# Optimization experiments

Hardware: AMD Instinct MI355X
Metric: run time of the kernel (lower is better)

The kernel has to match this reference:

```python
import math
import jax, jax.numpy as jnp
import numpy as np

IMG_SIZE = 2048
STRIDE = 8
NUM_CLASSES = 80
TOPK = 1000
CONF_THRESH = 0.05
NMS_THRESH = 0.6
CTR_CLAMP = 32.0
SCALE_CLAMP = math.log(1000.0 / 16)
ANCHOR_SIZES = np.array([[32,32],[64,32],[32,64],[64,64],[128,64],[64,128],[128,128],[256,128],[128,256]], dtype=np.float32)


def make_anchors():
    fmp = IMG_SIZE // STRIDE  # 256
    yy, xx = np.meshgrid(np.arange(fmp), np.arange(fmp), indexing='ij')
    xy = (np.stack([xx, yy], axis=-1).reshape(-1, 2).astype(np.float32) + 0.5) * STRIDE  # [fmp*fmp, 2]
    na = ANCHOR_SIZES.shape[0]
    xy = np.repeat(xy[:, None, :], na, axis=1)           # [fmp*fmp, na, 2]
    wh = np.tile(ANCHOR_SIZES[None, :, :], (fmp * fmp, 1, 1))  # [fmp*fmp, na, 2]
    return jnp.asarray(np.concatenate([xy, wh], axis=-1).reshape(-1, 4))  # [M, 4]


def setup_inputs() -> dict:
    key = jax.random.key(0)
    k1, k2 = jax.random.split(key)
    M = (IMG_SIZE // STRIDE) ** 2 * ANCHOR_SIZES.shape[0]
    cls_pred = jax.random.normal(k1, (M, NUM_CLASSES), dtype=jnp.float32) * 2.0 - 2.0
    reg_pred = jax.random.normal(k2, (M, 4), dtype=jnp.float32) * 0.5
    anchor_boxes = make_anchors()
    return {"cls_pred": cls_pred, "reg_pred": reg_pred, "anchor_boxes": anchor_boxes}


def decode_boxes(anchors, reg):
    # anchors, reg: [N, 4] (cx, cy, w, h) / (dx, dy, dw, dh)
    ctr_off = jnp.clip(reg[..., :2] * anchors[..., 2:], -CTR_CLAMP, CTR_CLAMP)
    ctr = anchors[..., :2] + ctr_off
    wh = anchors[..., 2:] * jnp.exp(jnp.minimum(reg[..., 2:], SCALE_CLAMP))
    return jnp.concatenate([ctr - 0.5 * wh, ctr + 0.5 * wh], axis=-1)


def iou_matrix(boxes):
    # boxes: [N, 4] x1y1x2y2 -> [N, N] IoU, matching the numpy NMS math
    x1, y1, x2, y2 = boxes[:, 0], boxes[:, 1], boxes[:, 2], boxes[:, 3]
    areas = (x2 - x1) * (y2 - y1)
    xx1 = jnp.maximum(x1[:, None], x1[None, :])
    yy1 = jnp.maximum(y1[:, None], y1[None, :])
    xx2 = jnp.minimum(x2[:, None], x2[None, :])
    yy2 = jnp.minimum(y2[:, None], y2[None, :])
    w = jnp.maximum(1e-10, xx2 - xx1)
    h = jnp.maximum(1e-10, yy2 - yy1)
    inter = w * h
    return inter / (areas[:, None] + areas[None, :] - inter + 1e-10)


def reference(cls_pred, reg_pred, anchor_boxes):
    # per-anchor best class score/label
    probs = jax.nn.sigmoid(cls_pred)                 # [M, C]
    scores_all = jnp.max(probs, axis=-1)             # [M]
    labels_all = jnp.argmax(probs, axis=-1)          # [M]
    # top-k filtering (scores sorted descending)
    scores, idx = jax.lax.top_k(scores_all, TOPK)    # [K]
    labels = labels_all[idx]
    reg = reg_pred[idx]
    anch = anchor_boxes[idx]
    # decode + normalize
    bboxes = jnp.clip(decode_boxes(anch, reg) / IMG_SIZE, 0.0, 1.0)  # [K, 4]
    valid = scores >= CONF_THRESH                    # conf filter as mask (fixed shape)
    # per-class greedy NMS: candidates are score-sorted, so greedy order = index order
    iou = iou_matrix(bboxes)                         # [K, K]
    same_cls = labels[:, None] == labels[None, :]    # [K, K]
    suppress_mat = (iou > NMS_THRESH) & same_cls     # j suppresses i if kept, same class, earlier
    idx_range = jnp.arange(TOPK)

    def body(i, keep):
        earlier_kept_overlap = jnp.any(keep & suppress_mat[:, i] & (idx_range < i))
        return keep.at[i].set(valid[i] & ~earlier_kept_overlap)

    keep = jax.lax.fori_loop(0, TOPK, body, jnp.zeros(TOPK, dtype=bool))
    return bboxes, scores, labels, keep
```

## Files before the change

kernel.cpp:

```cpp
#include <hip/hip_runtime.h>
#include <math.h>

#define M_ANCH   589824
#define NCLS     80
#define TOPK_N   1000
#define CAND_CAP 4096
#define NREP     16
#define NBIN     8192
#define KSHIFT   19

#define SCALE_CLAMP_F 4.135166556742356f
#define INV_IMG       (1.0f/2048.0f)

#define WS_H1R     0
#define WS_CNT     524288
#define WS_GBIN    524292
#define WS_MEMSET  524296
#define WS_CAND    524544
#define WS_BOXES   557312
#define WS_LABELS  573312
#define WS_VALID   577312
#define WS_SUP     581376
#define WS_MKEYS   712704

__device__ __forceinline__ unsigned fmap(unsigned b) {
    return (b & 0x80000000u) ? ~b : (b | 0x80000000u);
}
__device__ __forceinline__ unsigned funmap(unsigned k) {
    return (k & 0x80000000u) ? (k ^ 0x80000000u) : ~k;
}

__global__ __launch_bounds__(256) void k_rowmax(const float* __restrict__ cls,
                                                unsigned* __restrict__ mkeys,
                                                unsigned* __restrict__ h1r) {
    __shared__ float    cmax[256 * 21];
    __shared__ unsigned lh[NBIN / 2];
    int t = threadIdx.x;
    for (int b = t; b < NBIN / 2; b += 256) lh[b] = 0;

    const float4* p = (const float4*)cls + (size_t)blockIdx.x * (256 * 20);
#pragma unroll
    for (int i = 0; i < 20; ++i) {
        float4 v = p[i * 256 + t];
        float c = fmaxf(fmaxf(v.x, v.y), fmaxf(v.z, v.w));
        int cid = i * 256 + t;
        int row = cid / 20;
        int j   = cid - row * 20;
        cmax[row * 21 + j] = c;
    }
    __syncthreads();

    const float* rp = &cmax[t * 21];
    float m = -INFINITY;
#pragma unroll
    for (int j = 0; j < 20; ++j) m = fmaxf(m, rp[j]);
    unsigned key = fmap(__float_as_uint(m));
    mkeys[blockIdx.x * 256 + t] = key;
    unsigned bin = key >> KSHIFT;
    atomicAdd(&lh[bin >> 1], 1u << ((bin & 1) << 4));
    __syncthreads();

    unsigned rep = (blockIdx.x & (NREP - 1)) * NBIN;
    for (int b2 = t; b2 < NBIN / 2; b2 += 256) {
        unsigned c = lh[b2];
        unsigned c0 = c & 0xFFFFu, c1 = c >> 16;
        if (c0) atomicAdd(&h1r[rep + 2 * b2], c0);
        if (c1) atomicAdd(&h1r[rep + 2 * b2 + 1], c1);
    }
}

__global__ __launch_bounds__(1024) void k_find(const unsigned* __restrict__ h1r,
                                               unsigned* __restrict__ gbin) {
    __shared__ unsigned hist[NBIN];
    __shared__ unsigned csum[256];
    int t = threadIdx.x;
    for (int b = t; b < NBIN; b += 1024) {
        unsigned s = 0;
#pragma unroll
        for (int r = 0; r < NREP; ++r) s += h1r[r * NBIN + b];
        hist[b] = s;
    }
    __syncthreads();
    if (t < 256) {
        unsigned cs = 0;
        for (int k = 0; k < 32; ++k) cs += hist[t * 32 + k];
        csum[t] = cs;
    }
    __syncthreads();
    if (t == 0) {
        unsigned cum = 0, above = 0;
        int C = 0;
        for (int c = 255; c >= 0; --c) {
            if (cum + csum[c] >= TOPK_N || c == 0) { C = c; above = cum; break; }
            cum += csum[c];
        }
        int B = C * 32;
        unsigned cum2 = above;
        for (int b = C * 32 + 31; b >= C * 32; --b) {
            cum2 += hist[b];
            if (cum2 >= TOPK_N) { B = b; break; }
            if (b == C * 32) B = b;
        }
        *gbin = (B >= 1) ? (unsigned)(B - 1) : 0u;
    }
}

__global__ __launch_bounds__(256) void k_gather(const uint4* __restrict__ mk4,
                                                const unsigned* __restrict__ gbin,
                                                unsigned* __restrict__ cnt,
                                                unsigned long long* __restrict__ cand) {
    int tid = blockIdx.x * 256 + threadIdx.x;
    unsigned gb = *gbin;
    uint4 a = mk4[tid * 2];
    uint4 b4 = mk4[tid * 2 + 1];
    unsigned keys[8] = {a.x, a.y, a.z, a.w, b4.x, b4.y, b4.z, b4.w};
    int lc = 0;
    unsigned sel[8];
#pragma unroll
    for (int q = 0; q < 8; ++q)
        if ((keys[q] >> KSHIFT) >= gb) sel[lc++] = (unsigned)q;
    if (lc) {
        unsigned base = atomicAdd(cnt, (unsigned)lc);
        for (int q = 0; q < lc; ++q) {
            unsigned pos = base + (unsigned)q;
            if (pos < CAND_CAP) {
                unsigned i = (unsigned)tid * 8u + sel[q];
                float m = __uint_as_float(funmap(keys[sel[q]]));
                float e = (float)exp(-(double)m);
                float sc = 1.0f / (1.0f + e);
                cand[pos] = ((unsigned long long)__float_as_uint(sc) << 32)
                            | (unsigned)(~i);
            }
        }
    }
}

__global__ __launch_bounds__(256) void k_rank_decode(const unsigned* __restrict__ cnt,
                                                     const unsigned long long* __restrict__ cand,
                                                     const float* __restrict__ cls,
                                                     const float* __restrict__ reg,
                                                     const float* __restrict__ anch,
                                                     float* __restrict__ out,
                                                     float4* __restrict__ boxes_ws,
                                                     int* __restrict__ lab_ws,
                                                     int* __restrict__ val_ws) {
    __shared__ unsigned long long sh[CAND_CAP];
    int t = threadIdx.x;
    unsigned n = *cnt;
    if (n > CAND_CAP) n = CAND_CAP;
    for (int k = t; k < (int)n; k += 256) sh[k] = cand[k];
    __syncthreads();
    int k = blockIdx.x * 256 + t;
    if (k >= (int)n) return;
    unsigned long long key = sh[k];
    int rank = 0;
    for (int j = 0; j < (int)n; ++j) rank += (sh[j] > key) ? 1 : 0;
    if (rank >= TOPK_N) return;
    int r = rank;
    unsigned idx = ~(unsigned)(key & 0xFFFFFFFFull);
    float sc = __uint_as_float((unsigned)(key >> 32));
    const float4* rowp = (const float4*)(cls + (size_t)idx * NCLS);
    float best = -INFINITY;
    int lbl = 0;
#pragma unroll
    for (int c4 = 0; c4 < 20; ++c4) {
        float4 v = rowp[c4];
        if (v.x > best) { best = v.x; lbl = c4 * 4; }
        if (v.y > best) { best = v.y; lbl = c4 * 4 + 1; }
        if (v.z > best) { best = v.z; lbl = c4 * 4 + 2; }
        if (v.w > best) { best = v.w; lbl = c4 * 4 + 3; }
    }
    float4 rg = ((const float4*)reg)[idx];
    float4 an = ((const float4*)anch)[idx];
    float ox = fminf(fmaxf(rg.x * an.z, -32.0f), 32.0f);
    float oy = fminf(fmaxf(rg.y * an.w, -32.0f), 32.0f);
    float cx = an.x + ox, cy = an.y + oy;
    float w = an.z * expf(fminf(rg.z, SCALE_CLAMP_F));
    float h = an.w * expf(fminf(rg.w, SCALE_CLAMP_F));
    float x1 = fminf(fmaxf((cx - 0.5f * w) * INV_IMG, 0.0f), 1.0f);
    float y1 = fminf(fmaxf((cy - 0.5f * h) * INV_IMG, 0.0f), 1.0f);
    float x2 = fminf(fmaxf((cx + 0.5f * w) * INV_IMG, 0.0f), 1.0f);
    float y2 = fminf(fmaxf((cy + 0.5f * h) * INV_IMG, 0.0f), 1.0f);
    out[r * 4 + 0] = x1;
    out[r * 4 + 1] = y1;
    out[r * 4 + 2] = x2;
    out[r * 4 + 3] = y2;
    out[4 * TOPK_N + r] = sc;
    out[5 * TOPK_N + r] = (float)lbl;
    boxes_ws[r] = make_float4(x1, y1, x2, y2);
    lab_ws[r] = lbl;
    val_ws[r] = (sc >= 0.05f) ? 1 : 0;
}

__global__ __launch_bounds__(64) void k_sup(const float4* __restrict__ boxes,
                                            const int* __restrict__ labs,
                                            unsigned long long* __restrict__ supT) {
    int i = blockIdx.x;
    int lane = threadIdx.x;
    int cmax = i >> 6;
    float4 bi = boxes[i];
    float ai = (bi.z - bi.x) * (bi.w - bi.y);
    int li = labs[i];
    for (int c = 0; c <= cmax; ++c) {
        int j = c * 64 + lane;
        bool bit = false;
        if (j < TOPK_N) {
            float4 bj = boxes[j];
            float aj = (bj.z - bj.x) * (bj.w - bj.y);
            float xx1 = fmaxf(bi.x, bj.x), yy1 = fmaxf(bi.y, bj.y);
            float xx2 = fminf(bi.z, bj.z), yy2 = fminf(bi.w, bj.w);
            float w = fmaxf(1e-10f, xx2 - xx1);
            float h = fmaxf(1e-10f, yy2 - yy1);
            float inter = w * h;
            float iou = inter / (ai + aj - inter + 1e-10f);
            bit = (iou > 0.6f) && (labs[j] == li);
        }
        unsigned long long ball = __ballot(bit);
        if (lane == 0) supT[(size_t)c * 1024 + i] = ball;
    }
}

__global__ __launch_bounds__(64) void k_nms(const unsigned long long* __restrict__ supT,
                                            const int* __restrict__ val,
                                            float* __restrict__ out_keep) {
    int lane = threadIdx.x;
    unsigned long long kw[16];
    unsigned long long lowmask = (lane == 0) ? 0ull : (~0ull >> (64 - lane));
#pragma unroll
    for (int c = 0; c < 16; ++c) {
        int b = c * 64 + lane;
        bool inb = (b < TOPK_N);
        unsigned long long tmp[16];
#pragma unroll
        for (int w = 0; w <= c; ++w)
            tmp[w] = inb ? supT[(size_t)w * 1024 + b] : 0ull;
        bool v = inb && (val[b] != 0);
        bool ext = false;
#pragma unroll
        for (int w = 0; w < c; ++w) ext = ext || ((tmp[w] & kw[w]) != 0ull);
        unsigned long long m = tmp[c];
        unsigned long long inchunk = m & lowmask;
        bool mykeep;
        if (__ballot(inchunk != 0ull) == 0ull) {
            mykeep = v && !ext;
        } else {
            mykeep = false;
            for (int i = 0; i < 64; ++i) {
                unsigned long long ball = __ballot(mykeep);
                if (lane == i) mykeep = v && !ext && ((ball & inchunk) == 0ull);
            }
        }
        unsigned long long ball2 = __ballot(mykeep);
        kw[c] = ball2;
        if (inb) out_keep[b] = ((ball2 >> lane) & 1ull) ? 1.0f : 0.0f;
    }
}

extern "C" void kernel_launch(void* const* d_in, const int* in_sizes, int n_in,
                              void* d_out, int out_size, void* d_ws, size_t ws_size,
                              hipStream_t stream) {
    const float* cls  = (const float*)d_in[0];
    const float* reg  = (const float*)d_in[1];
    const float* anch = (const float*)d_in[2];
    float* out = (float*)d_out;
    char* ws = (char*)d_ws;

    unsigned* h1r  = (unsigned*)(ws + WS_H1R);
    unsigned* cnt  = (unsigned*)(ws + WS_CNT);
    unsigned* gbin = (unsigned*)(ws + WS_GBIN);
    unsigned long long* cand = (unsigned long long*)(ws + WS_CAND);
    float4* boxes = (float4*)(ws + WS_BOXES);
    int* labs     = (int*)(ws + WS_LABELS);
    int* valid    = (int*)(ws + WS_VALID);
    unsigned long long* supT = (unsigned long long*)(ws + WS_SUP);
    unsigned* mkeys = (unsigned*)(ws + WS_MKEYS);

    hipMemsetAsync(ws, 0, WS_MEMSET, stream);

    k_rowmax<<<M_ANCH / 256, 256, 0, stream>>>(cls, mkeys, h1r);
    k_find  <<<1, 1024, 0, stream>>>(h1r, gbin);
    k_gather<<<M_ANCH / (256 * 8), 256, 0, stream>>>((const uint4*)mkeys, gbin, cnt, cand);
    k_rank_decode<<<CAND_CAP / 256, 256, 0, stream>>>(cnt, cand, cls, reg, anch,
                                                      out, boxes, labs, valid);
    k_sup   <<<TOPK_N, 64, 0, stream>>>(boxes, labs, supT);
    k_nms   <<<1, 64, 0, stream>>>(supT, valid, out + 6 * TOPK_N);
}
```

Before: 368.6 us.

## Fuse histogram reduce/find and suppress/NMS via last-block ticket pattern

The single-block histogram reduction becomes a 32-block parallel reduction, and the last block to finish (picked with an atomic ticket) runs the threshold search. The suppression-matrix and greedy NMS kernels are merged the same way, with four rows per 256-thread block and the last block doing the NMS. This removes a kernel launch boundary in each pair and spreads the histogram reduction across many CUs. The cost is extra thread fences, an atomic counter that must be zeroed each call, and a serial tail run by whichever block finishes last.

```diff
diff --git a/kernel.cpp b/kernel.cpp
--- a/kernel.cpp
+++ b/kernel.cpp
@@ -15,13 +15,16 @@
 #define WS_H1R     0
 #define WS_CNT     524288
 #define WS_GBIN    524292
-#define WS_MEMSET  524296
+#define WS_TICK1   524296
+#define WS_TICK2   524300
+#define WS_MEMSET  524304
 #define WS_CAND    524544
 #define WS_BOXES   557312
 #define WS_LABELS  573312
 #define WS_VALID   577312
 #define WS_SUP     581376
 #define WS_MKEYS   712704
+#define WS_HRED    3072000
 
 __device__ __forceinline__ unsigned fmap(unsigned b) {
     return (b & 0x80000000u) ? ~b : (b | 0x80000000u);
@@ -69,19 +72,29 @@
     }
 }
 
-__global__ __launch_bounds__(1024) void k_find(const unsigned* __restrict__ h1r,
-                                               unsigned* __restrict__ gbin) {
+__global__ __launch_bounds__(256) void k_red_find(const unsigned* __restrict__ h1r,
+                                                  unsigned* __restrict__ hred,
+                                                  unsigned* __restrict__ ticket,
+                                                  unsigned* __restrict__ gbin) {
     __shared__ unsigned hist[NBIN];
     __shared__ unsigned csum[256];
+    __shared__ unsigned amLast;
     int t = threadIdx.x;
-    for (int b = t; b < NBIN; b += 1024) {
-        unsigned s = 0;
-#pragma unroll
-        for (int r = 0; r < NREP; ++r) s += h1r[r * NBIN + b];
-        hist[b] = s;
-    }
-    __syncthreads();
-    if (t < 256) {
+    int b = blockIdx.x * 256 + t;
+    unsigned s = 0;
+#pragma unroll
+    for (int r = 0; r < NREP; ++r) s += h1r[r * NBIN + b];
+    hred[b] = s;
+    __threadfence();
+    __syncthreads();
+    if (t == 0) amLast = (atomicAdd(ticket, 1u) == (NBIN / 256 - 1)) ? 1u : 0u;
+    __syncthreads();
+    if (!amLast) return;
+    __threadfence();
+
+    for (int i = t; i < NBIN; i += 256) hist[i] = hred[i];
+    __syncthreads();
+    {
         unsigned cs = 0;
         for (int k = 0; k < 32; ++k) cs += hist[t * 32 + k];
         csum[t] = cs;
@@ -96,10 +109,10 @@
         }
         int B = C * 32;
         unsigned cum2 = above;
-        for (int b = C * 32 + 31; b >= C * 32; --b) {
-            cum2 += hist[b];
-            if (cum2 >= TOPK_N) { B = b; break; }
-            if (b == C * 32) B = b;
+        for (int b2 = C * 32 + 31; b2 >= C * 32; --b2) {
+            cum2 += hist[b2];
+            if (cum2 >= TOPK_N) { B = b2; break; }
+            if (b2 == C * 32) B = b2;
         }
         *gbin = (B >= 1) ? (unsigned)(B - 1) : 0u;
     }
@@ -192,67 +205,77 @@
     val_ws[r] = (sc >= 0.05f) ? 1 : 0;
 }
 
-__global__ __launch_bounds__(64) void k_sup(const float4* __restrict__ boxes,
-                                            const int* __restrict__ labs,
-                                            unsigned long long* __restrict__ supT) {
-    int i = blockIdx.x;
-    int lane = threadIdx.x;
-    int cmax = i >> 6;
-    float4 bi = boxes[i];
-    float ai = (bi.z - bi.x) * (bi.w - bi.y);
-    int li = labs[i];
-    for (int c = 0; c <= cmax; ++c) {
-        int j = c * 64 + lane;
-        bool bit = false;
-        if (j < TOPK_N) {
-            float4 bj = boxes[j];
-            float aj = (bj.z - bj.x) * (bj.w - bj.y);
-            float xx1 = fmaxf(bi.x, bj.x), yy1 = fmaxf(bi.y, bj.y);
-            float xx2 = fminf(bi.z, bj.z), yy2 = fminf(bi.w, bj.w);
-            float w = fmaxf(1e-10f, xx2 - xx1);
-            float h = fmaxf(1e-10f, yy2 - yy1);
-            float inter = w * h;
-            float iou = inter / (ai + aj - inter + 1e-10f);
-            bit = (iou > 0.6f) && (labs[j] == li);
-        }
-        unsigned long long ball = __ballot(bit);
-        if (lane == 0) supT[(size_t)c * 1024 + i] = ball;
-    }
-}
-
-__global__ __launch_bounds__(64) void k_nms(const unsigned long long* __restrict__ supT,
-                                            const int* __restrict__ val,
-                                            float* __restrict__ out_keep) {
-    int lane = threadIdx.x;
-    unsigned long long kw[16];
-    unsigned long long lowmask = (lane == 0) ? 0ull : (~0ull >> (64 - lane));
-#pragma unroll
-    for (int c = 0; c < 16; ++c) {
-        int b = c * 64 + lane;
-        bool inb = (b < TOPK_N);
-        unsigned long long tmp[16];
-#pragma unroll
-        for (int w = 0; w <= c; ++w)
-            tmp[w] = inb ? supT[(size_t)w * 1024 + b] : 0ull;
-        bool v = inb && (val[b] != 0);
-        bool ext = false;
-#pragma unroll
-        for (int w = 0; w < c; ++w) ext = ext || ((tmp[w] & kw[w]) != 0ull);
-        unsigned long long m = tmp[c];
-        unsigned long long inchunk = m & lowmask;
-        bool mykeep;
-        if (__ballot(inchunk != 0ull) == 0ull) {
-            mykeep = v && !ext;
-        } else {
-            mykeep = false;
-            for (int i = 0; i < 64; ++i) {
-                unsigned long long ball = __ballot(mykeep);
-                if (lane == i) mykeep = v && !ext && ((ball & inchunk) == 0ull);
+__global__ __launch_bounds__(256) void k_sup_nms(const float4* __restrict__ boxes,
+                                                 const int* __restrict__ labs,
+                                                 unsigned long long* __restrict__ supT,
+                                                 unsigned* __restrict__ ticket,
+                                                 const int* __restrict__ val,
+                                                 float* __restrict__ out_keep) {
+    __shared__ unsigned amLast;
+    int t = threadIdx.x;
+    int i = blockIdx.x * 4 + (t >> 6);
+    int lane = t & 63;
+    if (i < TOPK_N) {
+        int cmax = i >> 6;
+        float4 bi = boxes[i];
+        float ai = (bi.z - bi.x) * (bi.w - bi.y);
+        int li = labs[i];
+        for (int c = 0; c <= cmax; ++c) {
+            int j = c * 64 + lane;
+            bool bit = false;
+            if (j < TOPK_N) {
+                float4 bj = boxes[j];
+                float aj = (bj.z - bj.x) * (bj.w - bj.y);
+                float xx1 = fmaxf(bi.x, bj.x), yy1 = fmaxf(bi.y, bj.y);
+                float xx2 = fminf(bi.z, bj.z), yy2 = fminf(bi.w, bj.w);
+                float w = fmaxf(1e-10f, xx2 - xx1);
+                float h = fmaxf(1e-10f, yy2 - yy1);
+                float inter = w * h;
+                float iou = inter / (ai + aj - inter + 1e-10f);
+                bit = (iou > 0.6f) && (labs[j] == li);
             }
-        }
-        unsigned long long ball2 = __ballot(mykeep);
-        kw[c] = ball2;
-        if (inb) out_keep[b] = ((ball2 >> lane) & 1ull) ? 1.0f : 0.0f;
+            unsigned long long ball = __ballot(bit);
+            if (lane == 0) supT[(size_t)c * 1024 + i] = ball;
+        }
+    }
+    __threadfence();
+    __syncthreads();
+    if (t == 0) amLast = (atomicAdd(ticket, 1u) == (TOPK_N / 4 - 1)) ? 1u : 0u;
+    __syncthreads();
+    if (!amLast) return;
+    __threadfence();
+
+    if (t < 64) {
+        unsigned long long kw[16];
+        unsigned long long lowmask = (lane == 0) ? 0ull : (~0ull >> (64 - lane));
+#pragma unroll
+        for (int c = 0; c < 16; ++c) {
+            int b = c * 64 + lane;
+            bool inb = (b < TOPK_N);
+            unsigned long long tmp[16];
+#pragma unroll
+            for (int w = 0; w <= c; ++w)
+                tmp[w] = inb ? supT[(size_t)w * 1024 + b] : 0ull;
+            bool v = inb && (val[b] != 0);
+            bool ext = false;
+#pragma unroll
+            for (int w = 0; w < c; ++w) ext = ext || ((tmp[w] & kw[w]) != 0ull);
+            unsigned long long m = tmp[c];
+            unsigned long long inchunk = m & lowmask;
+            bool mykeep;
+            if (__ballot(inchunk != 0ull) == 0ull) {
+                mykeep = v && !ext;
+            } else {
+                mykeep = false;
+                for (int ii = 0; ii < 64; ++ii) {
+                    unsigned long long ball = __ballot(mykeep);
+                    if (lane == ii) mykeep = v && !ext && ((ball & inchunk) == 0ull);
+                }
+            }
+            unsigned long long ball2 = __ballot(mykeep);
+            kw[c] = ball2;
+            if (inb) out_keep[b] = ((ball2 >> lane) & 1ull) ? 1.0f : 0.0f;
+        }
     }
 }
 
@@ -265,23 +288,26 @@
     float* out = (float*)d_out;
     char* ws = (char*)d_ws;
 
-    unsigned* h1r  = (unsigned*)(ws + WS_H1R);
-    unsigned* cnt  = (unsigned*)(ws + WS_CNT);
-    unsigned* gbin = (unsigned*)(ws + WS_GBIN);
+    unsigned* h1r   = (unsigned*)(ws + WS_H1R);
+    unsigned* cnt   = (unsigned*)(ws + WS_CNT);
+    unsigned* gbin  = (unsigned*)(ws + WS_GBIN);
+    unsigned* tick1 = (unsigned*)(ws + WS_TICK1);
+    unsigned* tick2 = (unsigned*)(ws + WS_TICK2);
     unsigned long long* cand = (unsigned long long*)(ws + WS_CAND);
     float4* boxes = (float4*)(ws + WS_BOXES);
     int* labs     = (int*)(ws + WS_LABELS);
     int* valid    = (int*)(ws + WS_VALID);
     unsigned long long* supT = (unsigned long long*)(ws + WS_SUP);
     unsigned* mkeys = (unsigned*)(ws + WS_MKEYS);
+    unsigned* hred  = (unsigned*)(ws + WS_HRED);
 
     hipMemsetAsync(ws, 0, WS_MEMSET, stream);
 
-    k_rowmax<<<M_ANCH / 256, 256, 0, stream>>>(cls, mkeys, h1r);
-    k_find  <<<1, 1024, 0, stream>>>(h1r, gbin);
-    k_gather<<<M_ANCH / (256 * 8), 256, 0, stream>>>((const uint4*)mkeys, gbin, cnt, cand);
+    k_rowmax  <<<M_ANCH / 256, 256, 0, stream>>>(cls, mkeys, h1r);
+    k_red_find<<<NBIN / 256, 256, 0, stream>>>(h1r, hred, tick1, gbin);
+    k_gather  <<<M_ANCH / (256 * 8), 256, 0, stream>>>((const uint4*)mkeys, gbin, cnt, cand);
     k_rank_decode<<<CAND_CAP / 256, 256, 0, stream>>>(cnt, cand, cls, reg, anch,
                                                       out, boxes, labs, valid);
-    k_sup   <<<TOPK_N, 64, 0, stream>>>(boxes, labs, supT);
-    k_nms   <<<1, 64, 0, stream>>>(supT, valid, out + 6 * TOPK_N);
-}
+    k_sup_nms <<<TOPK_N / 4, 256, 0, stream>>>(boxes, labs, supT, tick2,
+                                               valid, out + 6 * TOPK_N);
+}
```

New measurement: 368.8 us. About the same (+0.1%).
